# Kernel tuning notes

Measured on AMD Instinct MI355X. Metric: run time of the kernel, lower is better.

Reference implementation:

```python
import jax, jax.numpy as jnp
import numpy as np

W1 = 7          # half window
W2 = 2 * W1 + 1 # window size = 15
H = 4           # num heads
DH = 64         # head dim
DO = H * DH     # 256


def setup_inputs() -> dict:
    key = jax.random.key(0)
    ks = jax.random.split(key, 7)
    B, T, D = 2, 4096, 768
    s = 1.0 / np.sqrt(D).astype(np.float32)
    inputs = jax.random.normal(ks[0], (B, T, D), dtype=jnp.float32)
    Wq = jax.random.normal(ks[1], (DO, D), dtype=jnp.float32) * s
    bq = jax.random.normal(ks[2], (DO,), dtype=jnp.float32) * s
    Wv = jax.random.normal(ks[3], (DO, D), dtype=jnp.float32) * s
    bv = jax.random.normal(ks[4], (DO,), dtype=jnp.float32) * s
    pos_emb = jax.random.normal(ks[5], (W2, D), dtype=jnp.float32)
    return {"inputs": inputs, "Wq": Wq, "bq": bq, "Wv": Wv, "bv": bv, "pos_emb": pos_emb}


def reference(inputs, Wq, bq, Wv, bv, pos_emb):
    # Faithful to the torch module: k uses the *query* projection (source bug),
    # no softmax, no 1/sqrt(d) scaling.
    B, T, D = inputs.shape
    pad = jnp.pad(inputs, ((0, 0), (W1, W1), (0, 0)))  # [B, T+2*W1, D]
    # Project once on the padded sequence, then gather windows (linear ops
    # commute with the window gather; position bias added post-projection).
    q_pad = pad @ Wq.T + bq            # [B, T+2*W1, DO]
    v_pad = pad @ Wv.T + bv            # [B, T+2*W1, DO]
    pos_q = pos_emb @ Wq.T             # [W2, DO]  (query(window+pos) = query(window)+pos@Wq^T)
    pos_v = pos_emb @ Wv.T             # [W2, DO]
    idx = jnp.arange(T)[:, None] + jnp.arange(W2)[None, :]  # [T, W2]
    k = q_pad[:, idx] + pos_q          # [B, T, W2, DO]
    v = v_pad[:, idx] + pos_v          # [B, T, W2, DO]
    q = inputs @ Wq.T + bq             # [B, T, DO]
    qh = q.reshape(B, T, H, DH)
    kh = k.reshape(B, T, W2, H, DH)
    vh = v.reshape(B, T, W2, H, DH)
    scores = jnp.einsum('bthd,btwhd->bthw', qh, kh)   # [B, T, H, W2] (no softmax)
    ctx = jnp.einsum('bthw,btwhd->bthd', scores, vh)  # [B, T, H, DH]
    return ctx.reshape(B, T, DO)
```

## Files before the change

kernel.cpp:

```cpp
#include <hip/hip_runtime.h>

#define TPC   4110
#define MROWS 8220
#define MTOT  8235
#define MPAD  8320
#define KD    768

typedef __attribute__((ext_vector_type(8))) short short8;
typedef __attribute__((ext_vector_type(4))) float f32x4;

#define LOAD_LDS16(gp, lp)                                                   \
  __builtin_amdgcn_global_load_lds(                                          \
      (const __attribute__((address_space(1))) void*)(gp),                   \
      (__attribute__((address_space(3))) void*)(lp), 16, 0, 0)

__device__ inline unsigned bfr(float x) {
  unsigned u = __float_as_uint(x);
  return (u + 0x7FFFu + ((u >> 16) & 1u)) >> 16;
}
__device__ inline unsigned pack2(float a, float b) {
  return bfr(a) | (bfr(b) << 16);
}
__device__ inline float bflo(unsigned u) { return __uint_as_float(u << 16); }
__device__ inline float bfhi(unsigned u) { return __uint_as_float(u & 0xffff0000u); }

__global__ __launch_bounds__(256) void cast_ab(
    const float* __restrict__ inp, const float* __restrict__ Wq,
    const float* __restrict__ Wv, const float* __restrict__ pos,
    ushort* __restrict__ Abf, ushort* __restrict__ Wbf) {
  const int ACH = MPAD * 96;
  int gid = blockIdx.x * 256 + threadIdx.x;
  const float* src = nullptr;
  ushort* dst;
  if (gid < ACH) {
    int row = gid / 96, c = (gid - row * 96) * 8;
    dst = Abf + (size_t)row * KD + c;
    if (row < MROWS) {
      int b = row / TPC, t = row - b * TPC - 7;
      if (t >= 0 && t < 4096) src = inp + ((size_t)b * 4096 + t) * KD + c;
    } else if (row < MTOT) {
      src = pos + (size_t)(row - MROWS) * KD + c;
    }
  } else {
    int wid = gid - ACH;
    if (wid >= 512 * 96) return;
    int row = wid / 96, c = (wid - row * 96) * 8;
    dst = Wbf + (size_t)row * KD + c;
    src = (row < 256) ? Wq + (size_t)row * KD + c
                      : Wv + (size_t)(row - 256) * KD + c;
  }
  uint4 o;
  if (src) {
    float4 f0 = *(const float4*)src;
    float4 f1 = *(const float4*)(src + 4);
    o.x = pack2(f0.x, f0.y); o.y = pack2(f0.z, f0.w);
    o.z = pack2(f1.x, f1.y); o.w = pack2(f1.z, f1.w);
  } else {
    o.x = o.y = o.z = o.w = 0u;
  }
  *(uint4*)dst = o;
}

__global__ __launch_bounds__(256) void gemm_bf16(
    const ushort* __restrict__ Abf, const ushort* __restrict__ Wbf,
    const float* __restrict__ bq, const float* __restrict__ bv,
    ushort* __restrict__ q_out, ushort* __restrict__ v_out,
    ushort* __restrict__ pos_q, ushort* __restrict__ pos_v) {
  __shared__ ushort Al[64 * 64];
  __shared__ ushort Bl[128 * 64];
  const int tid = threadIdx.x;
  const int wave = tid >> 6, lane = tid & 63;
  const int ns = blockIdx.x;
  const int m0 = blockIdx.y * 64;
  const int wm = wave & 1, wn = wave >> 1;
  const int fr = lane & 15, quad = lane >> 4;

  const ushort* ag[2];
  #pragma unroll
  for (int i = 0; i < 2; i++) {
    int c = i * 256 + tid, row = c >> 3, kq = c & 7;
    ag[i] = Abf + (size_t)(m0 + row) * KD + ((kq ^ (row & 7)) * 8);
  }
  const ushort* bg[4];
  #pragma unroll
  for (int i = 0; i < 4; i++) {
    int c = i * 256 + tid, row = c >> 3, kq = c & 7;
    bg[i] = Wbf + (size_t)(ns * 128 + row) * KD + ((kq ^ (row & 7)) * 8);
  }
  ushort* al[2];
  ushort* bl[4];
  #pragma unroll
  for (int i = 0; i < 2; i++) al[i] = Al + (i * 256 + wave * 64) * 8;
  #pragma unroll
  for (int i = 0; i < 4; i++) bl[i] = Bl + (i * 256 + wave * 64) * 8;

  f32x4 acc[2][4];
  #pragma unroll
  for (int i = 0; i < 2; i++)
    #pragma unroll
    for (int j = 0; j < 4; j++) acc[i][j] = 0.0f;

  for (int k0 = 0; k0 < KD; k0 += 64) {
    #pragma unroll
    for (int i = 0; i < 2; i++) LOAD_LDS16(ag[i] + k0, al[i]);
    #pragma unroll
    for (int i = 0; i < 4; i++) LOAD_LDS16(bg[i] + k0, bl[i]);
    __syncthreads();
    short8 af[2][2], bf[2][4];
    #pragma unroll
    for (int ks = 0; ks < 2; ks++) {
      const int e = ((ks * 4 + quad) ^ (fr & 7)) * 8;
      #pragma unroll
      for (int i = 0; i < 2; i++)
        af[ks][i] = *(const short8*)(Al + (wm * 32 + i * 16 + fr) * 64 + e);
      #pragma unroll
      for (int j = 0; j < 4; j++)
        bf[ks][j] = *(const short8*)(Bl + (wn * 64 + j * 16 + fr) * 64 + e);
    }
    #pragma unroll
    for (int ks = 0; ks < 2; ks++)
      #pragma unroll
      for (int i = 0; i < 2; i++)
        #pragma unroll
        for (int j = 0; j < 4; j++)
          acc[i][j] = __builtin_amdgcn_mfma_f32_16x16x32_bf16(
              af[ks][i], bf[ks][j], acc[i][j], 0, 0, 0);
    __syncthreads();
  }

  const float* bias = (ns < 2) ? bq : bv;
  ushort* outp = (ns < 2) ? q_out : v_out;
  ushort* posp = (ns < 2) ? pos_q : pos_v;
  const int wbase = (ns & 1) * 128;
  #pragma unroll
  for (int j = 0; j < 4; j++) {
    const int colq = wbase + wn * 64 + j * 16 + fr;
    const int h = colq >> 6, d = colq & 63;
    const float bj = bias[colq];
    #pragma unroll
    for (int i = 0; i < 2; i++) {
      const int mb = m0 + wm * 32 + i * 16 + quad * 4;
      #pragma unroll
      for (int r = 0; r < 4; r++) {
        const int m = mb + r;
        if (m < MROWS) {
          int b = m / TPC, tp = m - b * TPC;
          outp[(((size_t)(b * 4 + h)) * TPC + tp) * 64 + d] =
              (ushort)bfr(acc[i][j][r] + bj);
        } else if (m < MTOT) {
          posp[(m - MROWS) * 256 + colq] = (ushort)bfr(acc[i][j][r]);
        }
      }
    }
  }
}

__global__ __launch_bounds__(256) void win_attn4(
    const ushort* __restrict__ q_out, const ushort* __restrict__ v_out,
    const ushort* __restrict__ pos_q, const ushort* __restrict__ pos_v,
    float* __restrict__ out) {
  __shared__ __align__(16) float ks[78][68];
  __shared__ __align__(16) float vs[78][68];
  __shared__ __align__(16) float pq[15][68];
  __shared__ __align__(16) float pv[15][68];
  const int tid = threadIdx.x;
  const int bh = blockIdx.x >> 6, tile = blockIdx.x & 63;
  const int b = bh >> 2, h = bh & 3;
  const int t0 = tile * 64;

  const size_t slab = (((size_t)(b * 4 + h)) * TPC + t0) * 64;
  for (int idx = tid; idx < 624; idx += 256) {
    int row = idx >> 3, c8 = (idx & 7) * 8;
    uint4 kc = *(const uint4*)(q_out + slab + idx * 8);
    ks[row][c8 + 0] = bflo(kc.x); ks[row][c8 + 1] = bfhi(kc.x);
    ks[row][c8 + 2] = bflo(kc.y); ks[row][c8 + 3] = bfhi(kc.y);
    ks[row][c8 + 4] = bflo(kc.z); ks[row][c8 + 5] = bfhi(kc.z);
    ks[row][c8 + 6] = bflo(kc.w); ks[row][c8 + 7] = bfhi(kc.w);
    uint4 vc = *(const uint4*)(v_out + slab + idx * 8);
    vs[row][c8 + 0] = bflo(vc.x); vs[row][c8 + 1] = bfhi(vc.x);
    vs[row][c8 + 2] = bflo(vc.y); vs[row][c8 + 3] = bfhi(vc.y);
    vs[row][c8 + 4] = bflo(vc.z); vs[row][c8 + 5] = bfhi(vc.z);
    vs[row][c8 + 6] = bflo(vc.w); vs[row][c8 + 7] = bfhi(vc.w);
  }
  if (tid < 120) {
    int row = tid >> 3, c8 = (tid & 7) * 8;
    uint4 qc = *(const uint4*)(pos_q + row * 256 + h * 64 + c8);
    pq[row][c8 + 0] = bflo(qc.x); pq[row][c8 + 1] = bfhi(qc.x);
    pq[row][c8 + 2] = bflo(qc.y); pq[row][c8 + 3] = bfhi(qc.y);
    pq[row][c8 + 4] = bflo(qc.z); pq[row][c8 + 5] = bfhi(qc.z);
    pq[row][c8 + 6] = bflo(qc.w); pq[row][c8 + 7] = bfhi(qc.w);
    uint4 vc = *(const uint4*)(pos_v + row * 256 + h * 64 + c8);
    pv[row][c8 + 0] = bflo(vc.x); pv[row][c8 + 1] = bfhi(vc.x);
    pv[row][c8 + 2] = bflo(vc.y); pv[row][c8 + 3] = bfhi(vc.y);
    pv[row][c8 + 4] = bflo(vc.z); pv[row][c8 + 5] = bfhi(vc.z);
    pv[row][c8 + 6] = bflo(vc.w); pv[row][c8 + 7] = bfhi(vc.w);
  }
  __syncthreads();

  const int tl = tid >> 2, qtr = tid & 3, d0 = qtr * 16;
  float4 qv[4];
  #pragma unroll
  for (int c = 0; c < 4; c++) qv[c] = *(float4*)&ks[tl + 7][d0 + c * 4];
  float4 ctx[4];
  #pragma unroll
  for (int c = 0; c < 4; c++) ctx[c] = make_float4(0.f, 0.f, 0.f, 0.f);

  #pragma unroll
  for (int w = 0; w < 15; w++) {
    float p = 0.f;
    #pragma unroll
    for (int c = 0; c < 4; c++) {
      float4 kk = *(float4*)&ks[tl + w][d0 + c * 4];
      float4 pp = *(float4*)&pq[w][d0 + c * 4];
      p += qv[c].x * (kk.x + pp.x) + qv[c].y * (kk.y + pp.y) +
           qv[c].z * (kk.z + pp.z) + qv[c].w * (kk.w + pp.w);
    }
    p += __shfl_xor(p, 1, 64);
    p += __shfl_xor(p, 2, 64);
    #pragma unroll
    for (int c = 0; c < 4; c++) {
      float4 vv = *(float4*)&vs[tl + w][d0 + c * 4];
      float4 pp = *(float4*)&pv[w][d0 + c * 4];
      ctx[c].x += p * (vv.x + pp.x);
      ctx[c].y += p * (vv.y + pp.y);
      ctx[c].z += p * (vv.z + pp.z);
      ctx[c].w += p * (vv.w + pp.w);
    }
  }
  size_t oo = ((size_t)(b * 4096 + t0 + tl)) * 256 + h * 64 + d0;
  #pragma unroll
  for (int c = 0; c < 4; c++) *(float4*)(out + oo + c * 4) = ctx[c];
}

extern "C" void kernel_launch(void* const* d_in, const int* in_sizes, int n_in,
                              void* d_out, int out_size, void* d_ws,
                              size_t ws_size, hipStream_t stream) {
  const float* inp = (const float*)d_in[0];
  const float* Wq  = (const float*)d_in[1];
  const float* bq  = (const float*)d_in[2];
  const float* Wv  = (const float*)d_in[3];
  const float* bv  = (const float*)d_in[4];
  const float* pos = (const float*)d_in[5];
  float* out = (float*)d_out;

  char* ws = (char*)d_ws;
  ushort* Abf   = (ushort*)ws;
  ushort* Wbf   = (ushort*)(ws + 12779520);
  ushort* q_out = (ushort*)(ws + 13565952);
  ushort* v_out = (ushort*)(ws + 17774592);
  ushort* pos_q = (ushort*)(ws + 21983232);
  ushort* pos_v = (ushort*)(ws + 21990912);

  const int cast_chunks = MPAD * 96 + 512 * 96;
  hipLaunchKernelGGL(cast_ab, dim3(cast_chunks / 256), dim3(256), 0, stream,
                     inp, Wq, Wv, pos, Abf, Wbf);
  hipLaunchKernelGGL(gemm_bf16, dim3(4, MPAD / 64), dim3(256), 0, stream,
                     Abf, Wbf, bq, bv, q_out, v_out, pos_q, pos_v);
  hipLaunchKernelGGL(win_attn4, dim3(2 * 4 * 64), dim3(256), 0, stream,
                     q_out, v_out, pos_q, pos_v, out);
}
```

Measured before the change: 109.6 us.

## Fuse activation fp32-to-bf16 cast into GEMM tile loads

Drops the separate pass that cast the padded activations to bf16. The GEMM now loads fp32 activation tiles straight into LDS, handling padding and pos_emb rows through pointer selection and a small zero page, and converts to bf16 while reading the MFMA fragments. This removes a full read-write of the activation matrix and its workspace buffer. In exchange the GEMM moves twice as many A-tile bytes into LDS, uses more LDS, and spends extra ALU on conversion inside the inner loop.

```diff
diff --git a/kernel.cpp b/kernel.cpp
--- a/kernel.cpp
+++ b/kernel.cpp
@@ -3,7 +3,6 @@
 #define TPC   4110
 #define MROWS 8220
 #define MTOT  8235
-#define MPAD  8320
 #define KD    768
 
 typedef __attribute__((ext_vector_type(8))) short short8;
@@ -21,52 +20,41 @@
 __device__ inline unsigned pack2(float a, float b) {
   return bfr(a) | (bfr(b) << 16);
 }
+__device__ inline unsigned pack2h(float a, float b) {
+  return ((__float_as_uint(a) + 0x8000u) >> 16) |
+         ((__float_as_uint(b) + 0x8000u) & 0xffff0000u);
+}
 __device__ inline float bflo(unsigned u) { return __uint_as_float(u << 16); }
 __device__ inline float bfhi(unsigned u) { return __uint_as_float(u & 0xffff0000u); }
 
-__global__ __launch_bounds__(256) void cast_ab(
-    const float* __restrict__ inp, const float* __restrict__ Wq,
-    const float* __restrict__ Wv, const float* __restrict__ pos,
-    ushort* __restrict__ Abf, ushort* __restrict__ Wbf) {
-  const int ACH = MPAD * 96;
+__global__ __launch_bounds__(256) void cast_w(
+    const float* __restrict__ Wq, const float* __restrict__ Wv,
+    ushort* __restrict__ Wbf, float* __restrict__ zpage) {
   int gid = blockIdx.x * 256 + threadIdx.x;
-  const float* src = nullptr;
-  ushort* dst;
-  if (gid < ACH) {
-    int row = gid / 96, c = (gid - row * 96) * 8;
-    dst = Abf + (size_t)row * KD + c;
-    if (row < MROWS) {
-      int b = row / TPC, t = row - b * TPC - 7;
-      if (t >= 0 && t < 4096) src = inp + ((size_t)b * 4096 + t) * KD + c;
-    } else if (row < MTOT) {
-      src = pos + (size_t)(row - MROWS) * KD + c;
-    }
-  } else {
-    int wid = gid - ACH;
-    if (wid >= 512 * 96) return;
-    int row = wid / 96, c = (wid - row * 96) * 8;
-    dst = Wbf + (size_t)row * KD + c;
-    src = (row < 256) ? Wq + (size_t)row * KD + c
-                      : Wv + (size_t)(row - 256) * KD + c;
-  }
+  if (gid == 0) {
+    *(uint4*)(zpage) = make_uint4(0, 0, 0, 0);
+    *(uint4*)(zpage + 4) = make_uint4(0, 0, 0, 0);
+    *(uint4*)(zpage + 8) = make_uint4(0, 0, 0, 0);
+    *(uint4*)(zpage + 12) = make_uint4(0, 0, 0, 0);
+  }
+  int row = gid / 96, c = (gid - row * 96) * 8;
+  const float* src = (row < 256) ? Wq + (size_t)row * KD + c
+                                 : Wv + (size_t)(row - 256) * KD + c;
+  float4 f0 = *(const float4*)src;
+  float4 f1 = *(const float4*)(src + 4);
   uint4 o;
-  if (src) {
-    float4 f0 = *(const float4*)src;
-    float4 f1 = *(const float4*)(src + 4);
-    o.x = pack2(f0.x, f0.y); o.y = pack2(f0.z, f0.w);
-    o.z = pack2(f1.x, f1.y); o.w = pack2(f1.z, f1.w);
-  } else {
-    o.x = o.y = o.z = o.w = 0u;
-  }
-  *(uint4*)dst = o;
-}
-
-__global__ __launch_bounds__(256) void gemm_bf16(
-    const ushort* __restrict__ Abf, const ushort* __restrict__ Wbf,
+  o.x = pack2(f0.x, f0.y); o.y = pack2(f0.z, f0.w);
+  o.z = pack2(f1.x, f1.y); o.w = pack2(f1.z, f1.w);
+  *(uint4*)(Wbf + (size_t)row * KD + c) = o;
+}
+
+__global__ __launch_bounds__(256) void gemm_fused(
+    const float* __restrict__ inp, const float* __restrict__ pos,
+    const float* __restrict__ zpage, const ushort* __restrict__ Wbf,
     const float* __restrict__ bq, const float* __restrict__ bv,
     ushort* __restrict__ q_out, ushort* __restrict__ v_out,
     ushort* __restrict__ pos_q, ushort* __restrict__ pos_v) {
-  __shared__ ushort Al[64 * 64];
+  __shared__ float  AlF[64 * 64];
   __shared__ ushort Bl[128 * 64];
   const int tid = threadIdx.x;
   const int wave = tid >> 6, lane = tid & 63;
@@ -75,11 +63,24 @@
   const int wm = wave & 1, wn = wave >> 1;
   const int fr = lane & 15, quad = lane >> 4;
 
-  const ushort* ag[2];
-  #pragma unroll
-  for (int i = 0; i < 2; i++) {
-    int c = i * 256 + tid, row = c >> 3, kq = c & 7;
-    ag[i] = Abf + (size_t)(m0 + row) * KD + ((kq ^ (row & 7)) * 8);
+  const float* agp[4];
+  bool aval[4];
+  #pragma unroll
+  for (int i = 0; i < 4; i++) {
+    int c = i * 256 + tid, row = c >> 4, kc = c & 15;
+    int m = m0 + row;
+    int woff = (kc ^ (row & 15)) * 4;
+    if (m < MROWS) {
+      int b = m / TPC, t = m - b * TPC - 7;
+      aval[i] = (t >= 0 && t < 4096);
+      agp[i] = aval[i] ? inp + ((size_t)b * 4096 + t) * KD + woff : zpage;
+    } else if (m < MTOT) {
+      aval[i] = true;
+      agp[i] = pos + (size_t)(m - MROWS) * KD + woff;
+    } else {
+      aval[i] = false;
+      agp[i] = zpage;
+    }
   }
   const ushort* bg[4];
   #pragma unroll
@@ -87,12 +88,13 @@
     int c = i * 256 + tid, row = c >> 3, kq = c & 7;
     bg[i] = Wbf + (size_t)(ns * 128 + row) * KD + ((kq ^ (row & 7)) * 8);
   }
-  ushort* al[2];
-  ushort* bl[4];
-  #pragma unroll
-  for (int i = 0; i < 2; i++) al[i] = Al + (i * 256 + wave * 64) * 8;
-  #pragma unroll
-  for (int i = 0; i < 4; i++) bl[i] = Bl + (i * 256 + wave * 64) * 8;
+  float* alw[4];
+  ushort* blw[4];
+  #pragma unroll
+  for (int i = 0; i < 4; i++) {
+    alw[i] = AlF + (i * 256 + wave * 64) * 4;
+    blw[i] = Bl + (i * 256 + wave * 64) * 8;
+  }
 
   f32x4 acc[2][4];
   #pragma unroll
@@ -102,17 +104,25 @@
 
   for (int k0 = 0; k0 < KD; k0 += 64) {
     #pragma unroll
-    for (int i = 0; i < 2; i++) LOAD_LDS16(ag[i] + k0, al[i]);
-    #pragma unroll
-    for (int i = 0; i < 4; i++) LOAD_LDS16(bg[i] + k0, bl[i]);
+    for (int i = 0; i < 4; i++) LOAD_LDS16(agp[i] + (aval[i] ? k0 : 0), alw[i]);
+    #pragma unroll
+    for (int i = 0; i < 4; i++) LOAD_LDS16(bg[i] + k0, blw[i]);
     __syncthreads();
+
     short8 af[2][2], bf[2][4];
     #pragma unroll
     for (int ks = 0; ks < 2; ks++) {
+      #pragma unroll
+      for (int i = 0; i < 2; i++) {
+        const int r = wm * 32 + i * 16 + fr;
+        float4 c0 = *(const float4*)(AlF + r * 64 + (((ks * 8) + quad * 2 + 0) ^ fr) * 4);
+        float4 c1 = *(const float4*)(AlF + r * 64 + (((ks * 8) + quad * 2 + 1) ^ fr) * 4);
+        union { unsigned u[4]; short8 s; } cv;
+        cv.u[0] = pack2h(c0.x, c0.y); cv.u[1] = pack2h(c0.z, c0.w);
+        cv.u[2] = pack2h(c1.x, c1.y); cv.u[3] = pack2h(c1.z, c1.w);
+        af[ks][i] = cv.s;
+      }
       const int e = ((ks * 4 + quad) ^ (fr & 7)) * 8;
-      #pragma unroll
-      for (int i = 0; i < 2; i++)
-        af[ks][i] = *(const short8*)(Al + (wm * 32 + i * 16 + fr) * 64 + e);
       #pragma unroll
       for (int j = 0; j < 4; j++)
         bf[ks][j] = *(const short8*)(Bl + (wn * 64 + j * 16 + fr) * 64 + e);
@@ -244,18 +254,17 @@
   float* out = (float*)d_out;
 
   char* ws = (char*)d_ws;
-  ushort* Abf   = (ushort*)ws;
-  ushort* Wbf   = (ushort*)(ws + 12779520);
-  ushort* q_out = (ushort*)(ws + 13565952);
-  ushort* v_out = (ushort*)(ws + 17774592);
-  ushort* pos_q = (ushort*)(ws + 21983232);
-  ushort* pos_v = (ushort*)(ws + 21990912);
-
-  const int cast_chunks = MPAD * 96 + 512 * 96;
-  hipLaunchKernelGGL(cast_ab, dim3(cast_chunks / 256), dim3(256), 0, stream,
-                     inp, Wq, Wv, pos, Abf, Wbf);
-  hipLaunchKernelGGL(gemm_bf16, dim3(4, MPAD / 64), dim3(256), 0, stream,
-                     Abf, Wbf, bq, bv, q_out, v_out, pos_q, pos_v);
+  ushort* Wbf   = (ushort*)ws;
+  float*  zpage = (float*)(ws + 786432);
+  ushort* q_out = (ushort*)(ws + 786688);
+  ushort* v_out = (ushort*)(ws + 4995328);
+  ushort* pos_q = (ushort*)(ws + 9203968);
+  ushort* pos_v = (ushort*)(ws + 9211648);
+
+  hipLaunchKernelGGL(cast_w, dim3(192), dim3(256), 0, stream,
+                     Wq, Wv, Wbf, zpage);
+  hipLaunchKernelGGL(gemm_fused, dim3(4, 129), dim3(256), 0, stream,
+                     inp, pos, zpage, Wbf, bq, bv, q_out, v_out, pos_q, pos_v);
   hipLaunchKernelGGL(win_attn4, dim3(2 * 4 * 64), dim3(256), 0, stream,
                      q_out, v_out, pos_q, pos_v, out);
 }
```

After: 111.4 us. Within noise of the previous version (+1.6%).
